# Kernel optimization log

Hardware: AMD Instinct MI355X
Metric: run time of the kernel (lower is better)

## Reference

```python
import jax, jax.numpy as jnp
import numpy as np

DIM = 768
HEADS = 8
DHEAD = 64
DEMB = HEADS * DHEAD  # 512
EPS = 1e-5


def layer_norm(x, g, b):
    mu = jnp.mean(x, axis=-1, keepdims=True)
    var = jnp.var(x, axis=-1, keepdims=True)
    return (x - mu) * jax.lax.rsqrt(var + EPS) * g + b


def setup_inputs() -> dict:
    key = jax.random.key(0)
    ks = jax.random.split(key, 9)
    b, t, n_src, n_ltn = 2, 4, 8192, 64
    inv = 1.0 / np.sqrt(DIM)
    return {
        "src": jax.random.normal(ks[0], (b, t, n_src, DIM), jnp.float32),
        "ltn": jax.random.normal(ks[1], (b, t, n_ltn, DIM), jnp.float32),
        "g_src": jnp.ones((DIM,), jnp.float32),
        "b_src": jnp.zeros((DIM,), jnp.float32),
        "g_ltn": jnp.ones((DIM,), jnp.float32),
        "b_ltn": jnp.zeros((DIM,), jnp.float32),
        # weights stored (in, out) so y = x @ W  (== torch Linear with W.T)
        "Wq": jax.random.normal(ks[2], (DIM, DEMB), jnp.float32) * inv,
        "Wkv": jax.random.normal(ks[3], (DIM, 2 * DEMB), jnp.float32) * inv,
        "Wo": jax.random.normal(ks[4], (DEMB, DIM), jnp.float32) * (1.0 / np.sqrt(DEMB)),
    }


def reference(src, ltn, g_src, b_src, g_ltn, b_ltn, Wq, Wkv, Wo):
    b, t, n_ltn, _ = ltn.shape
    n_src = src.shape[2]
    scale = DHEAD ** -0.5

    src_n = layer_norm(src, g_src, b_src)
    ltn_n = layer_norm(ltn, g_ltn, b_ltn)

    q = ltn_n @ Wq                                  # [b,t,nl,DEMB]
    ctx = jnp.concatenate([src_n, ltn_n], axis=-2)  # [b,t,ns+nl,DIM]
    kv = ctx @ Wkv                                  # [b,t,ns+nl,2*DEMB]
    k, v = jnp.split(kv, 2, axis=-1)

    def to_heads(x):  # b t n (h d) -> b h t n d
        B, T, N, _ = x.shape
        return x.reshape(B, T, N, HEADS, DHEAD).transpose(0, 3, 1, 2, 4)

    q, k, v = to_heads(q), to_heads(k), to_heads(v)

    attn = jnp.einsum('bhtid,bhtjd->bhtij', q, k) * scale
    attn = jax.nn.softmax(attn - jax.lax.stop_gradient(attn.max(axis=-1, keepdims=True)), axis=-1)
    out = jnp.einsum('bhtij,bhtjd->bhtid', attn, v)  # [b,h,t,nl,d]

    out = out.transpose(0, 2, 3, 1, 4).reshape(b, t, n_ltn, DEMB)
    return out @ Wo
```

## Files before the change

### kernel.cpp

```cpp
#include <hip/hip_runtime.h>
#include <hip/hip_bf16.h>
#include <type_traits>


#define N_SRC 8192
#define N_LTN 64
#define N_CTX 8256
#define NBT 8
#define MROWS 66048
#define DIMK 768
#define DEMB 512
#define NSPLIT 16
#define NTILES 65

typedef short short8 __attribute__((ext_vector_type(8)));
typedef float floatx4 __attribute__((ext_vector_type(4)));
typedef __attribute__((address_space(1))) void gvoid;
typedef __attribute__((address_space(3))) void lvoid;

__device__ inline ushort f2bf(float f) {
    union { float f; unsigned u; } v; v.f = f;
    unsigned u = v.u;
    return (ushort)((u + 0x7fffu + ((u >> 16) & 1u)) >> 16);
}

__global__ __launch_bounds__(256) void transpose_all(
        const float* __restrict__ Wkv, const float* __restrict__ Wq,
        const float* __restrict__ Wo, ushort* __restrict__ WkvT,
        ushort* __restrict__ WqT, ushort* __restrict__ WoT) {
    __shared__ ushort tile[64][65];
    int z = blockIdx.z;
    const float* in; ushort* out; int R, C;
    if (z == 0)      { in = Wkv; out = WkvT; R = 768; C = 1024; }
    else if (z == 1) { in = Wq;  out = WqT;  R = 768; C = 512;  }
    else             { in = Wo;  out = WoT;  R = 512; C = 768;  }
    int C0 = blockIdx.x * 64, R0 = blockIdx.y * 64;
    if (C0 >= C || R0 >= R) return;
    int tc = threadIdx.x & 63, tr4 = threadIdx.x >> 6;
#pragma unroll
    for (int j = 0; j < 16; j++) {
        int r = tr4 + j * 4;
        tile[r][tc] = f2bf(in[(size_t)(R0 + r) * C + C0 + tc]);
    }
    __syncthreads();
#pragma unroll
    for (int j = 0; j < 16; j++) {
        int c = tr4 + j * 4;
        out[(size_t)(C0 + c) * R + R0 + tc] = tile[tc][c];
    }
}

__global__ __launch_bounds__(256) void ln_kernel(
        const float* __restrict__ src, const float* __restrict__ ltn,
        const float* __restrict__ gs, const float* __restrict__ bs,
        const float* __restrict__ gl, const float* __restrict__ bl,
        ushort* __restrict__ ctx, ushort* __restrict__ qin) {
    int r = blockIdx.x * 4 + (threadIdx.x >> 6);
    int lane = threadIdx.x & 63;
    int bt = r / N_CTX;
    int i = r - bt * N_CTX;
    const float *x, *g, *b;
    int isl = (i >= N_SRC);
    if (!isl) { x = src + ((size_t)bt * N_SRC + i) * DIMK; g = gs; b = bs; }
    else      { x = ltn + ((size_t)bt * N_LTN + (i - N_SRC)) * DIMK; g = gl; b = bl; }
    float4 v[3]; float s = 0.f, s2 = 0.f;
#pragma unroll
    for (int t = 0; t < 3; t++) {
        float4 xv = *(const float4*)(x + t * 256 + lane * 4);
        v[t] = xv;
        s  += xv.x + xv.y + xv.z + xv.w;
        s2 += xv.x * xv.x + xv.y * xv.y + xv.z * xv.z + xv.w * xv.w;
    }
#pragma unroll
    for (int off = 32; off >= 1; off >>= 1) {
        s  += __shfl_xor(s,  off, 64);
        s2 += __shfl_xor(s2, off, 64);
    }
    float mu  = s * (1.0f / 768.0f);
    float var = s2 * (1.0f / 768.0f) - mu * mu;
    float rs  = rsqrtf(var + 1e-5f);
    ushort* crow = ctx + (size_t)r * DIMK;
    ushort* qrow = isl ? (qin + (size_t)(bt * N_LTN + (i - N_SRC)) * DIMK) : nullptr;
#pragma unroll
    for (int t = 0; t < 3; t++) {
        int idx = t * 256 + lane * 4;
        float4 gv = *(const float4*)(g + idx);
        float4 bv = *(const float4*)(b + idx);
        ushort4 u;
        u.x = f2bf((v[t].x - mu) * rs * gv.x + bv.x);
        u.y = f2bf((v[t].y - mu) * rs * gv.y + bv.y);
        u.z = f2bf((v[t].z - mu) * rs * gv.z + bv.z);
        u.w = f2bf((v[t].w - mu) * rs * gv.w + bv.w);
        *(ushort4*)(crow + idx) = u;
        if (isl) *(ushort4*)(qrow + idx) = u;
    }
}

template <typename CT>
__global__ __launch_bounds__(256) void gemm_bt(
        const ushort* __restrict__ A, const ushort* __restrict__ B,
        CT* __restrict__ C, int M, int N, int K) {
    __shared__ ushort lA[128 * 64];
    __shared__ ushort lB[128 * 64];
    int tid = threadIdx.x;
    int lane = tid & 63, wave = tid >> 6;
    int wm = wave >> 1, wn = wave & 1;
    int bn = blockIdx.x, bm = blockIdx.y;

    floatx4 acc[4][4];
#pragma unroll
    for (int mi = 0; mi < 4; mi++)
#pragma unroll
        for (int ni = 0; ni < 4; ni++) acc[mi][ni] = (floatx4){0.f, 0.f, 0.f, 0.f};

    int srow = lane >> 3;
    int schunk = (lane & 7) ^ srow;
    int quad = lane >> 4, lr = lane & 15;
    const int kiters = K >> 6;

    for (int kt = 0; kt < kiters; kt++) {
#pragma unroll
        for (int c2 = 0; c2 < 4; c2++) {
            int row = c2 * 32 + wave * 8 + srow;
            const ushort* gpA = A + ((size_t)(bm * 128 + row) * K + kt * 64 + schunk * 8);
            ushort* lpA = lA + (c2 * 32 + wave * 8) * 64 + lane * 8;
            __builtin_amdgcn_global_load_lds((gvoid*)gpA, (lvoid*)lpA, 16, 0, 0);
            const ushort* gpB = B + ((size_t)(bn * 128 + row) * K + kt * 64 + schunk * 8);
            ushort* lpB = lB + (c2 * 32 + wave * 8) * 64 + lane * 8;
            __builtin_amdgcn_global_load_lds((gvoid*)gpB, (lvoid*)lpB, 16, 0, 0);
        }
        __syncthreads();
#pragma unroll
        for (int ks = 0; ks < 2; ks++) {
            short8 av[4], bv[4];
            int slot = ((ks * 4 + quad) ^ (lane & 7)) * 8;
#pragma unroll
            for (int mi = 0; mi < 4; mi++)
                av[mi] = *(const short8*)(lA + (wm * 64 + mi * 16 + lr) * 64 + slot);
#pragma unroll
            for (int ni = 0; ni < 4; ni++)
                bv[ni] = *(const short8*)(lB + (wn * 64 + ni * 16 + lr) * 64 + slot);
#pragma unroll
            for (int mi = 0; mi < 4; mi++)
#pragma unroll
                for (int ni = 0; ni < 4; ni++)
                    acc[mi][ni] = __builtin_amdgcn_mfma_f32_16x16x32_bf16(
                        av[mi], bv[ni], acc[mi][ni], 0, 0, 0);
        }
        __syncthreads();
    }
#pragma unroll
    for (int mi = 0; mi < 4; mi++)
#pragma unroll
        for (int ni = 0; ni < 4; ni++)
#pragma unroll
            for (int r = 0; r < 4; r++) {
                int row = bm * 128 + wm * 64 + mi * 16 + quad * 4 + r;
                int col = bn * 128 + wn * 64 + ni * 16 + lr;
                float vv = acc[mi][ni][r];
                if constexpr (std::is_same<CT, ushort>::value)
                    C[(size_t)row * N + col] = f2bf(vv);
                else
                    C[(size_t)row * N + col] = vv;
            }
}

#define PR 136

__global__ __launch_bounds__(256) void attn_flash(
        const float* __restrict__ qf, const ushort* __restrict__ kvb,
        float* __restrict__ Op, float* __restrict__ ml) {
    __shared__ ushort lK[128 * 64];
    __shared__ ushort lVT[64 * PR];
    __shared__ ushort lP[64 * PR];

    int comb = blockIdx.x, split = blockIdx.y;
    int bt = comb >> 3, h = comb & 7;
    int tid = threadIdx.x;
    int w = tid >> 6, lane = tid & 63, quad = lane >> 4, lr = lane & 15;

    const ushort* kptr = kvb + (size_t)bt * N_CTX * 1024 + h * 64;
    const ushort* vptr = kptr + 512;

    short8 qa[2];
    {
        const float* p0 = qf + (size_t)(bt * 64 + w * 16 + lr) * DEMB + h * 64;
#pragma unroll
        for (int kc = 0; kc < 2; kc++) {
            const float* p = p0 + kc * 32 + quad * 8;
            float4 f0 = *(const float4*)p;
            float4 f1 = *(const float4*)(p + 4);
            short8 v;
            v[0] = f2bf(f0.x); v[1] = f2bf(f0.y); v[2] = f2bf(f0.z); v[3] = f2bf(f0.w);
            v[4] = f2bf(f1.x); v[5] = f2bf(f1.y); v[6] = f2bf(f1.z); v[7] = f2bf(f1.w);
            qa[kc] = v;
        }
    }

    floatx4 accO[4];
#pragma unroll
    for (int nt = 0; nt < 4; nt++) accO[nt] = (floatx4){0.f, 0.f, 0.f, 0.f};
    float m_run[4], l_run[4];
#pragma unroll
    for (int r = 0; r < 4; r++) { m_run[r] = -1e30f; l_run[r] = 0.f; }

    for (int t = split; t < NTILES; t += NSPLIT) {
        int kbase = t * 128;
        __syncthreads();

#pragma unroll
        for (int c2 = 0; c2 < 4; c2++) {
            int jloc = w * 32 + c2 * 8 + (lane >> 3);
            int chunk = (lane & 7) ^ ((lane >> 3) & 7);
            int jg = kbase + jloc; if (jg > N_CTX - 1) jg = N_CTX - 1;
            const ushort* gp = kptr + (size_t)jg * 1024 + chunk * 8;
            ushort* lp = lK + (w * 32 + c2 * 8) * 64 + lane * 8;
            __builtin_amdgcn_global_load_lds((gvoid*)gp, (lvoid*)lp, 16, 0, 0);
        }

        {
            int k0 = kbase + lane * 2;
            bool valid = (k0 + 1) < N_CTX;
            int k0c = valid ? k0 : (N_CTX - 2);
            const ushort* r0 = vptr + (size_t)k0c * 1024 + w * 16;
            const ushort* r1 = r0 + 1024;
            uint4 a0 = *(const uint4*)r0;
            uint4 a1 = *(const uint4*)(r0 + 8);
            uint4 b0 = *(const uint4*)r1;
            uint4 b1 = *(const uint4*)(r1 + 8);
            if (!valid) {
                a0 = make_uint4(0, 0, 0, 0); a1 = a0; b0 = a0; b1 = a0;
            }
            unsigned av8[8] = {a0.x, a0.y, a0.z, a0.w, a1.x, a1.y, a1.z, a1.w};
            unsigned bv8[8] = {b0.x, b0.y, b0.z, b0.w, b1.x, b1.y, b1.z, b1.w};
#pragma unroll
            for (int i = 0; i < 8; i++) {
                unsigned la = av8[i] & 0xffffu, ha = av8[i] >> 16;
                unsigned lb = bv8[i] & 0xffffu, hb = bv8[i] >> 16;
                *(unsigned*)(lVT + (w * 16 + 2 * i) * PR + lane * 2)     = la | (lb << 16);
                *(unsigned*)(lVT + (w * 16 + 2 * i + 1) * PR + lane * 2) = ha | (hb << 16);
            }
        }
        __syncthreads();

        floatx4 accS[8];
#pragma unroll
        for (int nt = 0; nt < 8; nt++) accS[nt] = (floatx4){0.f, 0.f, 0.f, 0.f};
#pragma unroll
        for (int kc = 0; kc < 2; kc++) {
#pragma unroll
            for (int nt = 0; nt < 8; nt++) {
                int kr = nt * 16 + lr;
                int slot = (kc * 4 + quad) ^ (kr & 7);
                short8 bv = *(const short8*)(lK + kr * 64 + slot * 8);
                accS[nt] = __builtin_amdgcn_mfma_f32_16x16x32_bf16(
                    qa[kc], bv, accS[nt], 0, 0, 0);
            }
        }

        float sc[8][4];
        float tmax[4] = {-1e30f, -1e30f, -1e30f, -1e30f};
#pragma unroll
        for (int nt = 0; nt < 8; nt++) {
            bool vk = (kbase + nt * 16 + lr) < N_CTX;
#pragma unroll
            for (int r = 0; r < 4; r++) {
                float s = vk ? accS[nt][r] * 0.125f : -1e30f;
                sc[nt][r] = s;
                tmax[r] = fmaxf(tmax[r], s);
            }
        }
#pragma unroll
        for (int r = 0; r < 4; r++) {
#pragma unroll
            for (int d = 1; d < 16; d <<= 1) tmax[r] = fmaxf(tmax[r], __shfl_xor(tmax[r], d, 64));
        }
        float alpha[4], lsum[4];
#pragma unroll
        for (int r = 0; r < 4; r++) {
            float mn = fmaxf(m_run[r], tmax[r]);
            alpha[r] = __expf(m_run[r] - mn);
            m_run[r] = mn;
            lsum[r] = 0.f;
        }

#pragma unroll
        for (int nt = 0; nt < 8; nt++) {
#pragma unroll
            for (int r = 0; r < 4; r++) {
                float p = __expf(sc[nt][r] - m_run[r]);
                lsum[r] += p;
                lP[(w * 16 + quad * 4 + r) * PR + nt * 16 + lr] = f2bf(p);
            }
        }
#pragma unroll
        for (int r = 0; r < 4; r++) {
#pragma unroll
            for (int d = 1; d < 16; d <<= 1) lsum[r] += __shfl_xor(lsum[r], d, 64);
            l_run[r] = l_run[r] * alpha[r] + lsum[r];
        }
#pragma unroll
        for (int nt = 0; nt < 4; nt++) {
            accO[nt][0] *= alpha[0]; accO[nt][1] *= alpha[1];
            accO[nt][2] *= alpha[2]; accO[nt][3] *= alpha[3];
        }

        short8 av[4];
#pragma unroll
        for (int kc = 0; kc < 4; kc++)
            av[kc] = *(const short8*)(lP + (w * 16 + lr) * PR + kc * 32 + quad * 8);
#pragma unroll
        for (int nt = 0; nt < 4; nt++)
#pragma unroll
            for (int kc = 0; kc < 4; kc++) {
                short8 bv = *(const short8*)(lVT + (nt * 16 + lr) * PR + kc * 32 + quad * 8);
                accO[nt] = __builtin_amdgcn_mfma_f32_16x16x32_bf16(av[kc], bv, accO[nt], 0, 0, 0);
            }
    }

    float* opb = Op + (size_t)(comb * NSPLIT + split) * 64 * 64;
#pragma unroll
    for (int nt = 0; nt < 4; nt++)
#pragma unroll
        for (int r = 0; r < 4; r++)
            opb[(w * 16 + quad * 4 + r) * 64 + nt * 16 + lr] = accO[nt][r];
    if (lr == 0) {
#pragma unroll
        for (int r = 0; r < 4; r++) {
            int row = w * 16 + quad * 4 + r;
            float* mlp = ml + ((size_t)(comb * NSPLIT + split) * 64 + row) * 2;
            mlp[0] = m_run[r]; mlp[1] = l_run[r];
        }
    }
}

__global__ __launch_bounds__(64) void attn_combine(
        const float* __restrict__ Op, const float* __restrict__ ml,
        ushort* __restrict__ outp) {
    int bx = blockIdx.x;
    int comb = bx >> 6, q = bx & 63;
    int bt = comb >> 3, h = comb & 7;
    int d = threadIdx.x;
    float M = -1e30f;
    for (int s = 0; s < NSPLIT; s++)
        M = fmaxf(M, ml[((size_t)(comb * NSPLIT + s) * 64 + q) * 2]);
    float L = 0.f, O = 0.f;
    for (int s = 0; s < NSPLIT; s++) {
        const float* p = ml + ((size_t)(comb * NSPLIT + s) * 64 + q) * 2;
        float wgt = __expf(p[0] - M);
        L = fmaf(wgt, p[1], L);
        O = fmaf(wgt, Op[((size_t)(comb * NSPLIT + s) * 64 + q) * 64 + d], O);
    }
    outp[(size_t)(bt * 64 + q) * DEMB + h * 64 + d] = f2bf(O / L);
}

extern "C" void kernel_launch(void* const* d_in, const int* in_sizes, int n_in,
                              void* d_out, int out_size, void* d_ws, size_t ws_size,
                              hipStream_t stream) {
    const float* src   = (const float*)d_in[0];
    const float* ltn   = (const float*)d_in[1];
    const float* g_src = (const float*)d_in[2];
    const float* b_src = (const float*)d_in[3];
    const float* g_ltn = (const float*)d_in[4];
    const float* b_ltn = (const float*)d_in[5];
    const float* Wq    = (const float*)d_in[6];
    const float* Wkv   = (const float*)d_in[7];
    const float* Wo    = (const float*)d_in[8];
    float* out = (float*)d_out;

    char* ws = (char*)d_ws;
    size_t off = 0;
    auto alloc = [&](size_t bytes) -> void* {
        void* p = ws + off;
        off += (bytes + 255) & ~(size_t)255;
        return p;
    };
    ushort* ctx  = (ushort*)alloc((size_t)MROWS * DIMK * 2);
    ushort* qin  = (ushort*)alloc((size_t)512 * DIMK * 2);
    ushort* WkvT = (ushort*)alloc((size_t)1024 * DIMK * 2);
    ushort* WqT  = (ushort*)alloc((size_t)512 * DIMK * 2);
    ushort* WoT  = (ushort*)alloc((size_t)768 * DEMB * 2);
    ushort* kvb  = (ushort*)alloc((size_t)MROWS * 1024 * 2);
    float*  qf   = (float*) alloc((size_t)512 * DEMB * 4);
    ushort* outp = (ushort*)alloc((size_t)512 * DEMB * 2);

    float* Op  = (float*)(void*)ctx;
    float* mlb = Op + (size_t)64 * NSPLIT * 64 * 64;

    transpose_all<<<dim3(16, 12, 3), 256, 0, stream>>>(Wkv, Wq, Wo, WkvT, WqT, WoT);

    ln_kernel<<<MROWS / 4, 256, 0, stream>>>(src, ltn, g_src, b_src, g_ltn, b_ltn, ctx, qin);

    gemm_bt<ushort><<<dim3(1024 / 128, MROWS / 128), 256, 0, stream>>>(
        ctx, WkvT, kvb, MROWS, 1024, DIMK);
    gemm_bt<float><<<dim3(512 / 128, 512 / 128), 256, 0, stream>>>(
        qin, WqT, qf, 512, 512, DIMK);

    attn_flash<<<dim3(64, NSPLIT), 256, 0, stream>>>(qf, kvb, Op, mlb);
    attn_combine<<<4096, 64, 0, stream>>>(Op, mlb, outp);

    gemm_bt<float><<<dim3(768 / 128, 512 / 128), 256, 0, stream>>>(
        outp, WoT, out, 512, 768, DEMB);
}
```

Before: 524.2 us.

## Add 256x256-tile pipelined GEMM for the KV projection

Replaces the 128x128-tile GEMM used for the large KV projection with a new 512-thread kernel that computes 256x256 output tiles. It double-buffers A and B in LDS using direct global-to-LDS loads, staged between MFMA phases with explicit barriers and priority hints, and remaps workgroups with a swizzle for cache locality. The larger tile raises operand reuse and cuts global traffic per FLOP. In exchange it uses much more LDS and registers per block, which can limit occupancy, and adds many barriers.

New measurement: 555.6 us. +6.0%, slower.

```diff
diff --git a/kernel.cpp b/kernel.cpp
--- a/kernel.cpp
+++ b/kernel.cpp
@@ -162,6 +162,136 @@
                     C[(size_t)row * N + col] = f2bf(vv);
                 else
                     C[(size_t)row * N + col] = vv;
+            }
+}
+
+template <typename CT>
+__global__ __launch_bounds__(512, 2) void gemm256_bt(
+        const ushort* __restrict__ A, const ushort* __restrict__ B,
+        CT* __restrict__ C, int M, int N, int K) {
+    __shared__ ushort lA[2][256 * 64];
+    __shared__ ushort lB[2][256 * 64];
+
+    int tid = threadIdx.x;
+    int lane = tid & 63, w = tid >> 6;
+    int wm = w >> 2, wn = w & 3;
+    int quad = lane >> 4, lr = lane & 15;
+
+    int ntile = N >> 8;
+    int nwg = gridDim.x;
+    int lin = blockIdx.x;
+    int swz = (lin & 7) * (nwg >> 3) + (lin >> 3);
+    int bn = swz % ntile, bm = swz / ntile;
+
+    const int kiters = K >> 6;
+
+    int srow = lane >> 3;
+    int schunk = (lane & 7) ^ srow;
+    const ushort* aG = A + (size_t)(bm * 256 + w * 8 + srow) * K + schunk * 8;
+    const ushort* bG = B + (size_t)(bn * 256 + w * 8 + srow) * K + schunk * 8;
+
+    auto stageA = [&](int nb, int h, int ktv) {
+#pragma unroll
+        for (int i = 0; i < 2; i++)
+            __builtin_amdgcn_global_load_lds(
+                (gvoid*)(aG + (size_t)(h * 128 + i * 64) * K + ktv * 64),
+                (lvoid*)(&lA[nb][(h * 128 + i * 64 + w * 8) * 64 + lane * 8]),
+                16, 0, 0);
+    };
+    auto stageB = [&](int nb, int h, int ktv) {
+#pragma unroll
+        for (int i = 0; i < 2; i++)
+            __builtin_amdgcn_global_load_lds(
+                (gvoid*)(bG + (size_t)(h * 128 + i * 64) * K + ktv * 64),
+                (lvoid*)(&lB[nb][(h * 128 + i * 64 + w * 8) * 64 + lane * 8]),
+                16, 0, 0);
+    };
+
+    floatx4 acc[8][4];
+#pragma unroll
+    for (int m = 0; m < 8; m++)
+#pragma unroll
+        for (int n = 0; n < 4; n++) acc[m][n] = (floatx4){0.f, 0.f, 0.f, 0.f};
+
+    const int arb = (wm * 128 + lr) * 64;
+    const int brb = (wn * 64 + lr) * 64;
+    const int sl0 = (quad ^ (lr & 7)) * 8;
+    const int sl1 = ((4 + quad) ^ (lr & 7)) * 8;
+
+    short8 af[4][2], bf[2][2];
+
+#define G256_FENCE asm volatile("" ::: "memory")
+#define G256_BAR do { G256_FENCE; __builtin_amdgcn_s_barrier(); G256_FENCE; } while (0)
+#define G256_DSA(mh_) do { _Pragma("unroll") \
+    for (int m2 = 0; m2 < 4; m2++) { \
+        af[m2][0] = *(const short8*)(lac + arb + ((mh_) * 64 + m2 * 16) * 64 + sl0); \
+        af[m2][1] = *(const short8*)(lac + arb + ((mh_) * 64 + m2 * 16) * 64 + sl1); } } while (0)
+#define G256_DSB(nh_) do { _Pragma("unroll") \
+    for (int n2 = 0; n2 < 2; n2++) { \
+        bf[n2][0] = *(const short8*)(lbc + brb + ((nh_) * 32 + n2 * 16) * 64 + sl0); \
+        bf[n2][1] = *(const short8*)(lbc + brb + ((nh_) * 32 + n2 * 16) * 64 + sl1); } } while (0)
+#define G256_MFMA(mh_, nh_) do { \
+    asm volatile("s_waitcnt lgkmcnt(0)"); \
+    __builtin_amdgcn_s_setprio(1); \
+    _Pragma("unroll") for (int kk = 0; kk < 2; kk++) \
+    _Pragma("unroll") for (int m2 = 0; m2 < 4; m2++) \
+    _Pragma("unroll") for (int n2 = 0; n2 < 2; n2++) \
+        acc[(mh_) * 4 + m2][(nh_) * 2 + n2] = __builtin_amdgcn_mfma_f32_16x16x32_bf16( \
+            af[m2][kk], bf[n2][kk], acc[(mh_) * 4 + m2][(nh_) * 2 + n2], 0, 0, 0); \
+    __builtin_amdgcn_s_setprio(0); } while (0)
+
+    stageA(0, 0, 0); stageA(0, 1, 0); stageB(0, 0, 0); stageB(0, 1, 0);
+
+    for (int kt = 0; kt < kiters; kt++) {
+        int c = kt & 1, nb = c ^ 1;
+        int ktn = (kt + 1 < kiters) ? kt + 1 : kt;
+        const ushort* lac = lA[c];
+        const ushort* lbc = lB[c];
+
+        stageA(nb, 0, ktn);
+        asm volatile("s_waitcnt vmcnt(2)" ::: "memory");
+        G256_BAR;
+        G256_DSA(0); G256_DSB(0);
+        G256_MFMA(0, 0);
+        G256_BAR;
+        G256_DSB(1);
+        stageA(nb, 1, ktn);
+        G256_BAR;
+        G256_MFMA(0, 1);
+        G256_BAR;
+        G256_DSA(1); G256_DSB(0);
+        stageB(nb, 0, ktn);
+        G256_BAR;
+        G256_MFMA(1, 0);
+        G256_BAR;
+        G256_DSB(1);
+        stageB(nb, 1, ktn);
+        G256_BAR;
+        G256_MFMA(1, 1);
+        G256_BAR;
+    }
+    asm volatile("s_waitcnt vmcnt(0)" ::: "memory");
+
+#undef G256_FENCE
+#undef G256_BAR
+#undef G256_DSA
+#undef G256_DSB
+#undef G256_MFMA
+
+    const int crb = bm * 256 + wm * 128 + quad * 4;
+    const int ccb = bn * 256 + wn * 64 + lr;
+#pragma unroll
+    for (int m = 0; m < 8; m++)
+#pragma unroll
+        for (int n = 0; n < 4; n++)
+#pragma unroll
+            for (int r = 0; r < 4; r++) {
+                int row = crb + m * 16 + r;
+                float vv = acc[m][n][r];
+                if constexpr (std::is_same<CT, ushort>::value)
+                    C[(size_t)row * N + ccb + n * 16] = f2bf(vv);
+                else
+                    C[(size_t)row * N + ccb + n * 16] = vv;
             }
 }
 
@@ -391,7 +521,7 @@
 
     ln_kernel<<<MROWS / 4, 256, 0, stream>>>(src, ltn, g_src, b_src, g_ltn, b_ltn, ctx, qin);
 
-    gemm_bt<ushort><<<dim3(1024 / 128, MROWS / 128), 256, 0, stream>>>(
+    gemm256_bt<ushort><<<dim3((MROWS / 256) * (1024 / 256)), 512, 0, stream>>>(
         ctx, WkvT, kvb, MROWS, 1024, DIMK);
     gemm_bt<float><<<dim3(512 / 128, 512 / 128), 256, 0, stream>>>(
         qin, WqT, qf, 512, 512, DIMK);
```
